# Kernel optimization log

Measured on AMD Instinct MI355X. Metric: run time of the kernel, lower is better.

## Reference

```python
import jax, jax.numpy as jnp
import numpy as np

INV_SQRT2 = 0.7071067811865476  # 1/sqrt(2)


def haar_wavelet_transform(x):
    length = x.shape[-1]
    max_level = int(np.log2(length))  # static, from shape
    approximations = []
    for _ in range(max_level):
        even = x[..., 0::2]
        odd = x[..., 1::2]
        cA = (even - odd) * INV_SQRT2
        cD = (even + odd) * INV_SQRT2
        approximations.append(cA)
        x = cD
    approximations.append(x)
    return tuple(approximations)


def setup_inputs() -> dict:
    key = jax.random.key(0)
    x = jax.random.normal(key, (64, 64, 16384), dtype=jnp.float32)
    return {"x": x}


def reference(x):
    return haar_wavelet_transform(x)
```

## Files before the change

kernel.cpp:

```cpp
#include <hip/hip_runtime.h>


typedef float f32x4 __attribute__((ext_vector_type(4)));
typedef float f32x2 __attribute__((ext_vector_type(2)));

constexpr int ROW_LEN = 16384;
constexpr int NROWS   = 64 * 64;
constexpr int NT      = 256;

__global__ __launch_bounds__(NT) void haar_kernel(const float* __restrict__ in,
                                                  float* __restrict__ out) {
    __shared__ __align__(16) float bufA[1024];
    __shared__ __align__(16) float bufB[512];

    const int row = blockIdx.x;
    const int tid = threadIdx.x;
    const float K = 0.70710678118654752440f;

    const f32x4* rin4 = (const f32x4*)(in + (size_t)row * ROW_LEN);

    f32x4* o1 = (f32x4*)(out + (size_t)row * 8192);
    f32x4* o2 = (f32x4*)(out + (size_t)NROWS * 8192  + (size_t)row * 4096);
    f32x2* o3 = (f32x2*)(out + (size_t)NROWS * 12288 + (size_t)row * 2048);
    float* o4 =          out + (size_t)NROWS * 14336 + (size_t)row * 1024;

    #pragma unroll
    for (int it = 0; it < ROW_LEN / (16 * NT); ++it) {
        const int tp = it * NT + tid;
        f32x4 v0 = __builtin_nontemporal_load(rin4 + 4 * tp + 0);
        f32x4 v1 = __builtin_nontemporal_load(rin4 + 4 * tp + 1);
        f32x4 v2 = __builtin_nontemporal_load(rin4 + 4 * tp + 2);
        f32x4 v3 = __builtin_nontemporal_load(rin4 + 4 * tp + 3);

        f32x4 ca1a = { (v0.x - v0.y) * K, (v0.z - v0.w) * K,
                       (v1.x - v1.y) * K, (v1.z - v1.w) * K };
        f32x4 ca1b = { (v2.x - v2.y) * K, (v2.z - v2.w) * K,
                       (v3.x - v3.y) * K, (v3.z - v3.w) * K };
        float d0 = (v0.x + v0.y) * K, d1 = (v0.z + v0.w) * K;
        float d2 = (v1.x + v1.y) * K, d3 = (v1.z + v1.w) * K;
        float d4 = (v2.x + v2.y) * K, d5 = (v2.z + v2.w) * K;
        float d6 = (v3.x + v3.y) * K, d7 = (v3.z + v3.w) * K;

        f32x4 ca2 = { (d0 - d1) * K, (d2 - d3) * K,
                      (d4 - d5) * K, (d6 - d7) * K };
        float e0 = (d0 + d1) * K, e1 = (d2 + d3) * K;
        float e2 = (d4 + d5) * K, e3 = (d6 + d7) * K;

        f32x2 ca3 = { (e0 - e1) * K, (e2 - e3) * K };
        float f0 = (e0 + e1) * K, f1 = (e2 + e3) * K;

        float ca4 = (f0 - f1) * K;
        float cd4 = (f0 + f1) * K;

        __builtin_nontemporal_store(ca1a, o1 + 2 * tp);
        __builtin_nontemporal_store(ca1b, o1 + 2 * tp + 1);
        __builtin_nontemporal_store(ca2,  o2 + tp);
        __builtin_nontemporal_store(ca3,  o3 + tp);
        __builtin_nontemporal_store(ca4,  o4 + tp);
        bufA[tp] = cd4;
    }
    __syncthreads();

    {
        f32x4 v = ((const f32x4*)bufA)[tid];
        f32x2 ca = { (v.x - v.y) * K, (v.z - v.w) * K };
        f32x2 cd = { (v.x + v.y) * K, (v.z + v.w) * K };
        f32x2* o5 = (f32x2*)(out + (size_t)NROWS * 15360 + (size_t)row * 512);
        o5[tid] = ca;
        ((f32x2*)bufB)[tid] = cd;
    }
    __syncthreads();

    if (tid < 128) {
        f32x4 v = ((const f32x4*)bufB)[tid];
        f32x2 ca = { (v.x - v.y) * K, (v.z - v.w) * K };
        f32x2 cd = { (v.x + v.y) * K, (v.z + v.w) * K };
        f32x2* o6 = (f32x2*)(out + (size_t)NROWS * 15872 + (size_t)row * 256);
        o6[tid] = ca;
        ((f32x2*)bufA)[tid] = cd;
    }
    __syncthreads();

    if (tid < 64) {
        f32x4 v = ((const f32x4*)bufA)[tid];
        f32x2 ca7 = { (v.x - v.y) * K, (v.z - v.w) * K };
        f32x2* o7 = (f32x2*)(out + (size_t)NROWS * 16128 + (size_t)row * 128);
        o7[tid] = ca7;
        float cd7a = (v.x + v.y) * K;
        float cd7b = (v.z + v.w) * K;

        float* o8 = out + (size_t)NROWS * 16256 + (size_t)row * 64;
        o8[tid] = (cd7a - cd7b) * K;
        float x = (cd7a + cd7b) * K;

        size_t chunk = (size_t)NROWS * 16320;
        #pragma unroll
        for (int L = 9; L <= 14; ++L) {
            const int n = ROW_LEN >> L;
            float even = __shfl(x, 2 * tid,     64);
            float odd  = __shfl(x, 2 * tid + 1, 64);
            float ca = (even - odd) * K;
            x        = (even + odd) * K;
            if (tid < n) out[chunk + (size_t)row * n + tid] = ca;
            chunk += (size_t)NROWS * n;
        }
        if (tid == 0) out[chunk + row] = x;
    }
}

extern "C" void kernel_launch(void* const* d_in, const int* in_sizes, int n_in,
                              void* d_out, int out_size, void* d_ws, size_t ws_size,
                              hipStream_t stream) {
    const float* x = (const float*)d_in[0];
    float* out = (float*)d_out;
    haar_kernel<<<dim3(NROWS), dim3(NT), 0, stream>>>(x, out);
}
```

Measured before the change: 450.8 us.

## Fuse three register-level Haar levels instead of four and drop nontemporal hints

The per-thread register stage now takes 8 inputs per iteration and computes three levels instead of four. Level 4 moves to a new shared-memory stage, so shared buffers double and one more barrier is added. Nontemporal loads and stores are replaced with plain loads and stores. This lowers register pressure and lets each thread issue narrower, more numerous memory operations, in exchange for extra LDS traffic, an additional sync, and the loss of the streaming cache hints.

```diff
diff --git a/kernel.cpp b/kernel.cpp
--- a/kernel.cpp
+++ b/kernel.cpp
@@ -10,8 +10,8 @@
 
 __global__ __launch_bounds__(NT) void haar_kernel(const float* __restrict__ in,
                                                   float* __restrict__ out) {
-    __shared__ __align__(16) float bufA[1024];
-    __shared__ __align__(16) float bufB[512];
+    __shared__ __align__(16) float bufA[2048];
+    __shared__ __align__(16) float bufB[1024];
 
     const int row = blockIdx.x;
     const int tid = threadIdx.x;
@@ -20,69 +20,77 @@
     const f32x4* rin4 = (const f32x4*)(in + (size_t)row * ROW_LEN);
 
     f32x4* o1 = (f32x4*)(out + (size_t)row * 8192);
-    f32x4* o2 = (f32x4*)(out + (size_t)NROWS * 8192  + (size_t)row * 4096);
-    f32x2* o3 = (f32x2*)(out + (size_t)NROWS * 12288 + (size_t)row * 2048);
-    float* o4 =          out + (size_t)NROWS * 14336 + (size_t)row * 1024;
+    f32x2* o2 = (f32x2*)(out + (size_t)NROWS * 8192  + (size_t)row * 4096);
+    float* o3 =          out + (size_t)NROWS * 12288 + (size_t)row * 2048;
 
     #pragma unroll
-    for (int it = 0; it < ROW_LEN / (16 * NT); ++it) {
+    for (int it = 0; it < ROW_LEN / (8 * NT); ++it) {
         const int tp = it * NT + tid;
-        f32x4 v0 = __builtin_nontemporal_load(rin4 + 4 * tp + 0);
-        f32x4 v1 = __builtin_nontemporal_load(rin4 + 4 * tp + 1);
-        f32x4 v2 = __builtin_nontemporal_load(rin4 + 4 * tp + 2);
-        f32x4 v3 = __builtin_nontemporal_load(rin4 + 4 * tp + 3);
+        f32x4 v0 = rin4[2 * tp];
+        f32x4 v1 = rin4[2 * tp + 1];
 
-        f32x4 ca1a = { (v0.x - v0.y) * K, (v0.z - v0.w) * K,
-                       (v1.x - v1.y) * K, (v1.z - v1.w) * K };
-        f32x4 ca1b = { (v2.x - v2.y) * K, (v2.z - v2.w) * K,
-                       (v3.x - v3.y) * K, (v3.z - v3.w) * K };
-        float d0 = (v0.x + v0.y) * K, d1 = (v0.z + v0.w) * K;
-        float d2 = (v1.x + v1.y) * K, d3 = (v1.z + v1.w) * K;
-        float d4 = (v2.x + v2.y) * K, d5 = (v2.z + v2.w) * K;
-        float d6 = (v3.x + v3.y) * K, d7 = (v3.z + v3.w) * K;
+        f32x4 ca1;
+        ca1.x = (v0.x - v0.y) * K;
+        ca1.y = (v0.z - v0.w) * K;
+        ca1.z = (v1.x - v1.y) * K;
+        ca1.w = (v1.z - v1.w) * K;
+        float d0 = (v0.x + v0.y) * K;
+        float d1 = (v0.z + v0.w) * K;
+        float d2 = (v1.x + v1.y) * K;
+        float d3 = (v1.z + v1.w) * K;
 
-        f32x4 ca2 = { (d0 - d1) * K, (d2 - d3) * K,
-                      (d4 - d5) * K, (d6 - d7) * K };
-        float e0 = (d0 + d1) * K, e1 = (d2 + d3) * K;
-        float e2 = (d4 + d5) * K, e3 = (d6 + d7) * K;
+        f32x2 ca2;
+        ca2.x = (d0 - d1) * K;
+        ca2.y = (d2 - d3) * K;
+        float e0 = (d0 + d1) * K;
+        float e1 = (d2 + d3) * K;
 
-        f32x2 ca3 = { (e0 - e1) * K, (e2 - e3) * K };
-        float f0 = (e0 + e1) * K, f1 = (e2 + e3) * K;
+        float ca3 = (e0 - e1) * K;
+        float cd3 = (e0 + e1) * K;
 
-        float ca4 = (f0 - f1) * K;
-        float cd4 = (f0 + f1) * K;
-
-        __builtin_nontemporal_store(ca1a, o1 + 2 * tp);
-        __builtin_nontemporal_store(ca1b, o1 + 2 * tp + 1);
-        __builtin_nontemporal_store(ca2,  o2 + tp);
-        __builtin_nontemporal_store(ca3,  o3 + tp);
-        __builtin_nontemporal_store(ca4,  o4 + tp);
-        bufA[tp] = cd4;
+        o1[tp]   = ca1;
+        o2[tp]   = ca2;
+        o3[tp]   = ca3;
+        bufA[tp] = cd3;
     }
     __syncthreads();
 
     {
-        f32x4 v = ((const f32x4*)bufA)[tid];
+        f32x2* o4 = (f32x2*)(out + (size_t)NROWS * 14336 + (size_t)row * 1024);
+        #pragma unroll
+        for (int p = 0; p < 2; ++p) {
+            const int idx = p * NT + tid;
+            f32x4 v = ((const f32x4*)bufA)[idx];
+            f32x2 ca = { (v.x - v.y) * K, (v.z - v.w) * K };
+            f32x2 cd = { (v.x + v.y) * K, (v.z + v.w) * K };
+            o4[idx] = ca;
+            ((f32x2*)bufB)[idx] = cd;
+        }
+    }
+    __syncthreads();
+
+    {
+        f32x4 v = ((const f32x4*)bufB)[tid];
         f32x2 ca = { (v.x - v.y) * K, (v.z - v.w) * K };
         f32x2 cd = { (v.x + v.y) * K, (v.z + v.w) * K };
         f32x2* o5 = (f32x2*)(out + (size_t)NROWS * 15360 + (size_t)row * 512);
         o5[tid] = ca;
+        ((f32x2*)bufA)[tid] = cd;
+    }
+    __syncthreads();
+
+    if (tid < 128) {
+        f32x4 v = ((const f32x4*)bufA)[tid];
+        f32x2 ca = { (v.x - v.y) * K, (v.z - v.w) * K };
+        f32x2 cd = { (v.x + v.y) * K, (v.z + v.w) * K };
+        f32x2* o6 = (f32x2*)(out + (size_t)NROWS * 15872 + (size_t)row * 256);
+        o6[tid] = ca;
         ((f32x2*)bufB)[tid] = cd;
     }
     __syncthreads();
 
-    if (tid < 128) {
+    if (tid < 64) {
         f32x4 v = ((const f32x4*)bufB)[tid];
-        f32x2 ca = { (v.x - v.y) * K, (v.z - v.w) * K };
-        f32x2 cd = { (v.x + v.y) * K, (v.z + v.w) * K };
-        f32x2* o6 = (f32x2*)(out + (size_t)NROWS * 15872 + (size_t)row * 256);
-        o6[tid] = ca;
-        ((f32x2*)bufA)[tid] = cd;
-    }
-    __syncthreads();
-
-    if (tid < 64) {
-        f32x4 v = ((const f32x4*)bufA)[tid];
         f32x2 ca7 = { (v.x - v.y) * K, (v.z - v.w) * K };
         f32x2* o7 = (f32x2*)(out + (size_t)NROWS * 16128 + (size_t)row * 128);
         o7[tid] = ca7;
```

After: 430.0 us. 1.05x faster.
